# Kernel tuning notes

Hardware: AMD Instinct MI355X
Metric: run time of the kernel (lower is better)

The kernel has to match this reference:

```python
import jax, jax.numpy as jnp
import numpy as np

T, B, C = 1024, 8, 1024
H, K, P = 16, 7, 3  # num_heads, kernel_size, padding_l
R = C // H


def setup_inputs() -> dict:
    key = jax.random.key(0)
    k1, k2, k3, k4 = jax.random.split(key, 4)
    x = jax.random.normal(k1, (T, B, C), dtype=jnp.float32)
    # weight_linear: Linear(C -> H*K) with bias
    lim = 1.0 / np.sqrt(C)
    W_lin = jax.random.uniform(k2, (H * K, C), minval=-lim, maxval=lim, dtype=jnp.float32)
    b_lin = jax.random.uniform(k3, (H * K,), minval=-lim, maxval=lim, dtype=jnp.float32)
    conv_bias = jnp.zeros((C,), dtype=jnp.float32)
    return {"x": x, "W_lin": W_lin, "b_lin": b_lin, "conv_bias": conv_bias}


def reference(x, W_lin, b_lin, conv_bias):
    # per-position dynamic filters: (T, B, H*K)
    w = jnp.einsum('tbc,oc->tbo', x, W_lin) + b_lin
    # weight_softmax=True, renorm_padding=False: softmax over kernel dim
    w = jax.nn.softmax(w.reshape(T * B * H, K), axis=-1)
    # (T, B*H, K) -> (B*H, T, K)
    w = w.reshape(T, B * H, K).transpose(1, 0, 2)
    # x as (B*H, T, R)
    xv = x.reshape(T, B * H, R).transpose(1, 0, 2)
    # band-matrix bmm == sliding window: out[t] = sum_k w[t,k] * x[t - P + k]
    x_pad = jnp.pad(xv, ((0, 0), (P, K - 1 - P), (0, 0)))
    windows = jnp.stack([x_pad[:, k:k + T] for k in range(K)], axis=2)  # (BH, T, K, R)
    out = jnp.einsum('btk,btkr->btr', w, windows)  # (BH, T, R)
    out = out.transpose(1, 0, 2).reshape(T, B, C)
    return out + conv_bias[None, None, :]
```

## Files before the change

### kernel.cpp

```cpp
#include <hip/hip_runtime.h>
#include <stdint.h>

#define T_DIM 1024
#define B_DIM 8
#define C_DIM 1024
#define H_DIM 16
#define K_SZ  7
#define P_PAD 3
#define O_DIM (H_DIM * K_SZ)
#define TB    (T_DIM * B_DIM)

typedef __attribute__((ext_vector_type(8))) short bf16x8;
typedef __attribute__((ext_vector_type(4))) float f32x4;
typedef __attribute__((ext_vector_type(4))) uint32_t u32x4;

union FragU { uint32_t u[4]; bf16x8 v; };

__device__ inline uint32_t pk_bf16(float a, float b) {
  uint32_t ua = __float_as_uint(a), ub = __float_as_uint(b);
  ua += 0x7FFFu + ((ua >> 16) & 1u);
  ub += 0x7FFFu + ((ub >> 16) & 1u);
  return (ua >> 16) | (ub & 0xFFFF0000u);
}

__device__ inline bf16x8 load_bf16x8_cvt(const float* __restrict__ p) {
  float4 lo = *reinterpret_cast<const float4*>(p);
  float4 hi = *reinterpret_cast<const float4*>(p + 4);
  FragU f;
  f.u[0] = pk_bf16(lo.x, lo.y);
  f.u[1] = pk_bf16(lo.z, lo.w);
  f.u[2] = pk_bf16(hi.x, hi.y);
  f.u[3] = pk_bf16(hi.z, hi.w);
  return f.v;
}

__device__ inline void bar_lds() {
  __builtin_amdgcn_sched_barrier(0);
  asm volatile("s_waitcnt lgkmcnt(0)" ::: "memory");
  __builtin_amdgcn_s_barrier();
  __builtin_amdgcn_sched_barrier(0);
}

__global__ __launch_bounds__(256) void prep_wfrag_kernel(
    const float* __restrict__ Wl, uint16_t* __restrict__ Wf) {
  const int t  = blockIdx.x * 256 + threadIdx.x;
  const int f  = t >> 6;
  const int l  = t & 63;
  const int ks = f / 7;
  const int nf = f - ks * 7;
  const int row = nf * 16 + (l & 15);
  const int kb  = ks * 32 + (l >> 4) * 8;
  bf16x8 v = load_bf16x8_cvt(Wl + (size_t)row * C_DIM + kb);
  *reinterpret_cast<bf16x8*>(Wf + (size_t)t * 8) = v;
}

template <bool PREPPED>
__global__ __launch_bounds__(1024, 4) void fused_pipe_kernel(
    const float* __restrict__ x, const float* __restrict__ Wl,
    const uint16_t* __restrict__ Wf, const float* __restrict__ bl,
    const float* __restrict__ cb, float* __restrict__ out) {
  __shared__ char  ring[32 * 2048];
  __shared__ float part[2][16][116];
  __shared__ float wsm[16][17][8];

  const int tid  = threadIdx.x;
  const int wv   = tid >> 6;
  const int lane = tid & 63;
  const int l15  = lane & 15;
  const int oct  = lane >> 4;

  const int bid = blockIdx.x;
  const int xcd = bid & 7;
  const int r8  = bid >> 3;
  const int b   = r8 >> 2;
  const int t0  = (xcd * 4 + (r8 & 3)) * 32;

  auto stage_write = [&](int task, int gbase) {
    const int q   = task >> 7;
    const int c16 = task & 127;
    const int g   = min(max(gbase + q, 0), T_DIM - 1);
    const float* __restrict__ src =
        x + ((size_t)(g * B_DIM + b)) * C_DIM + c16 * 8;
    float4 v0 = *reinterpret_cast<const float4*>(src);
    float4 v1 = *reinterpret_cast<const float4*>(src + 4);
    FragU f;
    f.u[0] = pk_bf16(v0.x, v0.y);
    f.u[1] = pk_bf16(v0.z, v0.w);
    f.u[2] = pk_bf16(v1.x, v1.y);
    f.u[3] = pk_bf16(v1.z, v1.w);
    const int dst = (g & 31) * 2048 + ((c16 * 16) ^ ((g & 7) << 4));
    *reinterpret_cast<bf16x8*>(ring + dst) = f.v;
  };

  auto mfma_phase = [&](int wbase) {
    if (wv < 14) {
      const int kh = (wv >= 7) ? 1 : 0;
      const int nf = wv - kh * 7;
      f32x4 acc = (f32x4)(0.f);
      const int ag   = wbase + l15;
      const char* ab = ring + (ag & 31) * 2048;
      const int axor = (ag & 7) << 4;
#pragma unroll
      for (int s = 0; s < 16; ++s) {
        const int ksg = kh * 16 + s;
        bf16x8 a = *reinterpret_cast<const bf16x8*>(
            ab + ((ksg * 64 + oct * 16) ^ axor));
        bf16x8 bf;
        if (PREPPED)
          bf = *reinterpret_cast<const bf16x8*>(
              Wf + ((size_t)((ksg * 7 + nf) * 64) + lane) * 8);
        else
          bf = load_bf16x8_cvt(Wl + (size_t)(nf * 16 + l15) * C_DIM + ksg * 32 + oct * 8);
        acc = __builtin_amdgcn_mfma_f32_16x16x32_bf16(a, bf, acc, 0, 0, 0);
      }
#pragma unroll
      for (int rr = 0; rr < 4; ++rr)
        part[kh][oct * 4 + rr][nf * 16 + l15] = acc[rr];
    }
  };

  auto softmax_phase = [&]() {
    if (tid < 256) {
      const int row = tid >> 4;
      const int h   = tid & 15;
      float lg[7];
      float m = -1e30f;
#pragma unroll
      for (int j = 0; j < 7; ++j) {
        const int c = h * 7 + j;
        float s_ = part[0][row][c] + part[1][row][c] + bl[c];
        lg[j] = s_;
        m = fmaxf(m, s_);
      }
      float s = 0.f;
#pragma unroll
      for (int j = 0; j < 7; ++j) { lg[j] = __expf(lg[j] - m); s += lg[j]; }
      const float inv = 1.0f / s;
#pragma unroll
      for (int j = 0; j < 7; ++j) wsm[row][h][j] = lg[j] * inv;
    }
  };

  auto conv_phase = [&](int wbase) {
    const int row  = wv;
    const int gout = wbase + row;
    float okf[7];
    int slotb[7], sxor[7];
#pragma unroll
    for (int j = 0; j < 7; ++j) {
      const int tp = gout + j - P_PAD;
      okf[j] = (tp >= 0 && tp < T_DIM) ? 1.f : 0.f;
      const int g = min(max(tp, 0), T_DIM - 1);
      slotb[j] = (g & 31) * 2048;
      sxor[j]  = (g & 7) << 4;
    }
    float* __restrict__ obase = out + ((size_t)(gout * B_DIM + b)) * C_DIM;
#pragma unroll
    for (int ii = 0; ii < 2; ++ii) {
      const int ch0  = ii * 512 + lane * 8;
      const int head = ch0 >> 6;
      float4 w0 = *reinterpret_cast<const float4*>(&wsm[row][head][0]);
      float4 w1 = *reinterpret_cast<const float4*>(&wsm[row][head][4]);
      const float wj[7] = {w0.x, w0.y, w0.z, w0.w, w1.x, w1.y, w1.z};
      float4 c0 = *reinterpret_cast<const float4*>(cb + ch0);
      float4 c1 = *reinterpret_cast<const float4*>(cb + ch0 + 4);
      float a0 = c0.x, a1 = c0.y, a2 = c0.z, a3 = c0.w;
      float a4 = c1.x, a5 = c1.y, a6 = c1.z, a7 = c1.w;
#pragma unroll
      for (int j = 0; j < 7; ++j) {
        const float w = wj[j] * okf[j];
        const u32x4 d = *reinterpret_cast<const u32x4*>(
            ring + slotb[j] + ((ch0 * 2) ^ sxor[j]));
        a0 += w * __uint_as_float(d.x << 16);
        a1 += w * __uint_as_float(d.x & 0xffff0000u);
        a2 += w * __uint_as_float(d.y << 16);
        a3 += w * __uint_as_float(d.y & 0xffff0000u);
        a4 += w * __uint_as_float(d.z << 16);
        a5 += w * __uint_as_float(d.z & 0xffff0000u);
        a6 += w * __uint_as_float(d.w << 16);
        a7 += w * __uint_as_float(d.w & 0xffff0000u);
      }
      *reinterpret_cast<float4*>(obase + ch0)     = make_float4(a0, a1, a2, a3);
      *reinterpret_cast<float4*>(obase + ch0 + 4) = make_float4(a4, a5, a6, a7);
    }
  };

#pragma unroll
  for (int it = 0; it < 3; ++it) {
    const int task = tid + it * 1024;
    if (task < 22 * 128) stage_write(task, t0 - 3);
  }
  bar_lds();

  float4 pf0, pf1, pf2, pf3;
  {
    const int q0 = tid >> 7, c0_ = tid & 127;
    const int g0 = min(t0 + 19 + q0, T_DIM - 1);
    const float* __restrict__ s0 =
        x + ((size_t)(g0 * B_DIM + b)) * C_DIM + c0_ * 8;
    pf0 = *reinterpret_cast<const float4*>(s0);
    pf1 = *reinterpret_cast<const float4*>(s0 + 4);
    const int t2 = tid + 1024;
    const int q1 = t2 >> 7, c1_ = t2 & 127;
    const int g1 = min(t0 + 19 + q1, T_DIM - 1);
    const float* __restrict__ s1 =
        x + ((size_t)(g1 * B_DIM + b)) * C_DIM + c1_ * 8;
    pf2 = *reinterpret_cast<const float4*>(s1);
    pf3 = *reinterpret_cast<const float4*>(s1 + 4);
  }

  mfma_phase(t0);
  bar_lds();
  softmax_phase();
  bar_lds();
  conv_phase(t0);
  bar_lds();

  {
    const int q0 = tid >> 7, c0_ = tid & 127;
    const int g0 = min(t0 + 19 + q0, T_DIM - 1);
    FragU f;
    f.u[0] = pk_bf16(pf0.x, pf0.y);
    f.u[1] = pk_bf16(pf0.z, pf0.w);
    f.u[2] = pk_bf16(pf1.x, pf1.y);
    f.u[3] = pk_bf16(pf1.z, pf1.w);
    *reinterpret_cast<bf16x8*>(
        ring + (g0 & 31) * 2048 + ((c0_ * 16) ^ ((g0 & 7) << 4))) = f.v;
    const int t2 = tid + 1024;
    const int q1 = t2 >> 7, c1_ = t2 & 127;
    const int g1 = min(t0 + 19 + q1, T_DIM - 1);
    FragU f2;
    f2.u[0] = pk_bf16(pf2.x, pf2.y);
    f2.u[1] = pk_bf16(pf2.z, pf2.w);
    f2.u[2] = pk_bf16(pf3.x, pf3.y);
    f2.u[3] = pk_bf16(pf3.z, pf3.w);
    *reinterpret_cast<bf16x8*>(
        ring + (g1 & 31) * 2048 + ((c1_ * 16) ^ ((g1 & 7) << 4))) = f2.v;
  }
  bar_lds();

  mfma_phase(t0 + 16);
  bar_lds();
  softmax_phase();
  bar_lds();
  conv_phase(t0 + 16);
}

extern "C" void kernel_launch(void* const* d_in, const int* in_sizes, int n_in,
                              void* d_out, int out_size, void* d_ws, size_t ws_size,
                              hipStream_t stream) {
  const float* x  = (const float*)d_in[0];
  const float* Wl = (const float*)d_in[1];
  const float* bl = (const float*)d_in[2];
  const float* cb = (const float*)d_in[3];
  float* out = (float*)d_out;

  const bool prepped = ws_size >= 262144;

  if (prepped) {
    uint16_t* wf = (uint16_t*)d_ws;
    prep_wfrag_kernel<<<(32 * 7 * 64) / 256, 256, 0, stream>>>(Wl, wf);
    fused_pipe_kernel<true><<<256, 1024, 0, stream>>>(x, Wl, wf, bl, cb, out);
  } else {
    fused_pipe_kernel<false><<<256, 1024, 0, stream>>>(x, Wl, nullptr, bl, cb, out);
  }
}
```

Measured before the change: 29.67 us.

## Drop weight prep kernel and keep W fragments in registers across phases

Removes the separate weight-prep launch. Each MFMA wave now loads and converts its 16 W_lin fragments into registers once at kernel start and reuses them for both 16-row MFMA phases. The single MFMA accumulator chain is split into two to shorten dependency latency. The conv phase uses packed float2 math and nontemporal stores, and the first barrier is moved after the prefetch loads. The cost is 16 bf16x8 registers per thread, which could hurt occupancy at 1024-thread blocks, plus redundant W conversion in every block.

```diff
diff --git a/kernel.cpp b/kernel.cpp
--- a/kernel.cpp
+++ b/kernel.cpp
@@ -12,6 +12,7 @@
 
 typedef __attribute__((ext_vector_type(8))) short bf16x8;
 typedef __attribute__((ext_vector_type(4))) float f32x4;
+typedef __attribute__((ext_vector_type(2))) float f32x2;
 typedef __attribute__((ext_vector_type(4))) uint32_t u32x4;
 
 union FragU { uint32_t u[4]; bf16x8 v; };
@@ -34,6 +35,13 @@
   return f.v;
 }
 
+__device__ inline f32x2 up2(uint32_t u) {
+  f32x2 r;
+  r.x = __uint_as_float(u << 16);
+  r.y = __uint_as_float(u & 0xffff0000u);
+  return r;
+}
+
 __device__ inline void bar_lds() {
   __builtin_amdgcn_sched_barrier(0);
   asm volatile("s_waitcnt lgkmcnt(0)" ::: "memory");
@@ -41,24 +49,10 @@
   __builtin_amdgcn_sched_barrier(0);
 }
 
-__global__ __launch_bounds__(256) void prep_wfrag_kernel(
-    const float* __restrict__ Wl, uint16_t* __restrict__ Wf) {
-  const int t  = blockIdx.x * 256 + threadIdx.x;
-  const int f  = t >> 6;
-  const int l  = t & 63;
-  const int ks = f / 7;
-  const int nf = f - ks * 7;
-  const int row = nf * 16 + (l & 15);
-  const int kb  = ks * 32 + (l >> 4) * 8;
-  bf16x8 v = load_bf16x8_cvt(Wl + (size_t)row * C_DIM + kb);
-  *reinterpret_cast<bf16x8*>(Wf + (size_t)t * 8) = v;
-}
-
-template <bool PREPPED>
 __global__ __launch_bounds__(1024, 4) void fused_pipe_kernel(
     const float* __restrict__ x, const float* __restrict__ Wl,
-    const uint16_t* __restrict__ Wf, const float* __restrict__ bl,
-    const float* __restrict__ cb, float* __restrict__ out) {
+    const float* __restrict__ bl, const float* __restrict__ cb,
+    float* __restrict__ out) {
   __shared__ char  ring[32 * 2048];
   __shared__ float part[2][16][116];
   __shared__ float wsm[16][17][8];
@@ -74,6 +68,16 @@
   const int r8  = bid >> 3;
   const int b   = r8 >> 2;
   const int t0  = (xcd * 4 + (r8 & 3)) * 32;
+
+  const int kh = (wv >= 7) ? 1 : 0;
+  const int nf = (wv < 14) ? (wv - kh * 7) : 0;
+  bf16x8 bfr[16];
+  if (wv < 14) {
+    const float* __restrict__ wp =
+        Wl + (size_t)(nf * 16 + l15) * C_DIM + kh * 512 + oct * 8;
+#pragma unroll
+    for (int s = 0; s < 16; ++s) bfr[s] = load_bf16x8_cvt(wp + s * 32);
+  }
 
   auto stage_write = [&](int task, int gbase) {
     const int q   = task >> 7;
@@ -94,28 +98,27 @@
 
   auto mfma_phase = [&](int wbase) {
     if (wv < 14) {
-      const int kh = (wv >= 7) ? 1 : 0;
-      const int nf = wv - kh * 7;
-      f32x4 acc = (f32x4)(0.f);
+      f32x4 acc0 = (f32x4)(0.f), acc1 = (f32x4)(0.f);
       const int ag   = wbase + l15;
       const char* ab = ring + (ag & 31) * 2048;
       const int axor = (ag & 7) << 4;
 #pragma unroll
-      for (int s = 0; s < 16; ++s) {
+      for (int s = 0; s < 8; ++s) {
         const int ksg = kh * 16 + s;
         bf16x8 a = *reinterpret_cast<const bf16x8*>(
             ab + ((ksg * 64 + oct * 16) ^ axor));
-        bf16x8 bf;
-        if (PREPPED)
-          bf = *reinterpret_cast<const bf16x8*>(
-              Wf + ((size_t)((ksg * 7 + nf) * 64) + lane) * 8);
-        else
-          bf = load_bf16x8_cvt(Wl + (size_t)(nf * 16 + l15) * C_DIM + ksg * 32 + oct * 8);
-        acc = __builtin_amdgcn_mfma_f32_16x16x32_bf16(a, bf, acc, 0, 0, 0);
+        acc0 = __builtin_amdgcn_mfma_f32_16x16x32_bf16(a, bfr[s], acc0, 0, 0, 0);
+      }
+#pragma unroll
+      for (int s = 8; s < 16; ++s) {
+        const int ksg = kh * 16 + s;
+        bf16x8 a = *reinterpret_cast<const bf16x8*>(
+            ab + ((ksg * 64 + oct * 16) ^ axor));
+        acc1 = __builtin_amdgcn_mfma_f32_16x16x32_bf16(a, bfr[s], acc1, 0, 0, 0);
       }
 #pragma unroll
       for (int rr = 0; rr < 4; ++rr)
-        part[kh][oct * 4 + rr][nf * 16 + l15] = acc[rr];
+        part[kh][oct * 4 + rr][nf * 16 + l15] = acc0[rr] + acc1[rr];
     }
   };
 
@@ -144,16 +147,6 @@
   auto conv_phase = [&](int wbase) {
     const int row  = wv;
     const int gout = wbase + row;
-    float okf[7];
-    int slotb[7], sxor[7];
-#pragma unroll
-    for (int j = 0; j < 7; ++j) {
-      const int tp = gout + j - P_PAD;
-      okf[j] = (tp >= 0 && tp < T_DIM) ? 1.f : 0.f;
-      const int g = min(max(tp, 0), T_DIM - 1);
-      slotb[j] = (g & 31) * 2048;
-      sxor[j]  = (g & 7) << 4;
-    }
     float* __restrict__ obase = out + ((size_t)(gout * B_DIM + b)) * C_DIM;
 #pragma unroll
     for (int ii = 0; ii < 2; ++ii) {
@@ -161,27 +154,35 @@
       const int head = ch0 >> 6;
       float4 w0 = *reinterpret_cast<const float4*>(&wsm[row][head][0]);
       float4 w1 = *reinterpret_cast<const float4*>(&wsm[row][head][4]);
-      const float wj[7] = {w0.x, w0.y, w0.z, w0.w, w1.x, w1.y, w1.z};
-      float4 c0 = *reinterpret_cast<const float4*>(cb + ch0);
-      float4 c1 = *reinterpret_cast<const float4*>(cb + ch0 + 4);
-      float a0 = c0.x, a1 = c0.y, a2 = c0.z, a3 = c0.w;
-      float a4 = c1.x, a5 = c1.y, a6 = c1.z, a7 = c1.w;
+      float wj[7] = {w0.x, w0.y, w0.z, w0.w, w1.x, w1.y, w1.z};
 #pragma unroll
       for (int j = 0; j < 7; ++j) {
-        const float w = wj[j] * okf[j];
+        const int tp = gout + j - P_PAD;
+        if (tp < 0 || tp >= T_DIM) wj[j] = 0.f;
+      }
+      f32x2 a0, a1, a2, a3;
+      {
+        float4 c0 = *reinterpret_cast<const float4*>(cb + ch0);
+        float4 c1 = *reinterpret_cast<const float4*>(cb + ch0 + 4);
+        a0.x = c0.x; a0.y = c0.y; a1.x = c0.z; a1.y = c0.w;
+        a2.x = c1.x; a2.y = c1.y; a3.x = c1.z; a3.y = c1.w;
+      }
+#pragma unroll
+      for (int j = 0; j < 7; ++j) {
+        const int g = min(max(gout + j - P_PAD, 0), T_DIM - 1);
         const u32x4 d = *reinterpret_cast<const u32x4*>(
-            ring + slotb[j] + ((ch0 * 2) ^ sxor[j]));
-        a0 += w * __uint_as_float(d.x << 16);
-        a1 += w * __uint_as_float(d.x & 0xffff0000u);
-        a2 += w * __uint_as_float(d.y << 16);
-        a3 += w * __uint_as_float(d.y & 0xffff0000u);
-        a4 += w * __uint_as_float(d.z << 16);
-        a5 += w * __uint_as_float(d.z & 0xffff0000u);
-        a6 += w * __uint_as_float(d.w << 16);
-        a7 += w * __uint_as_float(d.w & 0xffff0000u);
-      }
-      *reinterpret_cast<float4*>(obase + ch0)     = make_float4(a0, a1, a2, a3);
-      *reinterpret_cast<float4*>(obase + ch0 + 4) = make_float4(a4, a5, a6, a7);
+            ring + (g & 31) * 2048 + ((ch0 * 2) ^ ((g & 7) << 4)));
+        f32x2 w2; w2.x = wj[j]; w2.y = wj[j];
+        a0 += w2 * up2(d.x);
+        a1 += w2 * up2(d.y);
+        a2 += w2 * up2(d.z);
+        a3 += w2 * up2(d.w);
+      }
+      f32x4 o0, o1;
+      o0[0] = a0.x; o0[1] = a0.y; o0[2] = a1.x; o0[3] = a1.y;
+      o1[0] = a2.x; o1[1] = a2.y; o1[2] = a3.x; o1[3] = a3.y;
+      __builtin_nontemporal_store(o0, reinterpret_cast<f32x4*>(obase + ch0));
+      __builtin_nontemporal_store(o1, reinterpret_cast<f32x4*>(obase + ch0 + 4));
     }
   };
 
@@ -190,7 +191,6 @@
     const int task = tid + it * 1024;
     if (task < 22 * 128) stage_write(task, t0 - 3);
   }
-  bar_lds();
 
   float4 pf0, pf1, pf2, pf3;
   {
@@ -208,6 +208,7 @@
     pf2 = *reinterpret_cast<const float4*>(s1);
     pf3 = *reinterpret_cast<const float4*>(s1 + 4);
   }
+  bar_lds();
 
   mfma_phase(t0);
   bar_lds();
@@ -255,13 +256,5 @@
   const float* cb = (const float*)d_in[3];
   float* out = (float*)d_out;
 
-  const bool prepped = ws_size >= 262144;
-
-  if (prepped) {
-    uint16_t* wf = (uint16_t*)d_ws;
-    prep_wfrag_kernel<<<(32 * 7 * 64) / 256, 256, 0, stream>>>(Wl, wf);
-    fused_pipe_kernel<true><<<256, 1024, 0, stream>>>(x, Wl, wf, bl, cb, out);
-  } else {
-    fused_pipe_kernel<false><<<256, 1024, 0, stream>>>(x, Wl, nullptr, bl, cb, out);
-  }
-}
+  fused_pipe_kernel<<<256, 1024, 0, stream>>>(x, Wl, bl, cb, out);
+}
```

New measurement: 35.00 us. 18.0% more time.
